# Kernel tuning notes

Hardware: AMD Instinct MI355X
Metric: run time of the kernel (lower is better)

Reference implementation:

```python
import jax, jax.numpy as jnp
import numpy as np

N_NODES = 100000


def _gcn_aggregate(x, edge_index):
    """Symmetric-normalized GCN aggregation with self-loops (PyG gcn_norm).
    Returns A_hat @ x where A_hat = D^-1/2 (A + I) D^-1/2.
    """
    n = x.shape[0]
    row, col = edge_index[0], edge_index[1]          # messages flow row -> col
    loop = jnp.arange(n, dtype=edge_index.dtype)
    src = jnp.concatenate([row, loop])
    dst = jnp.concatenate([col, loop])
    # degree at target nodes (includes self-loop weight 1)
    deg = jax.ops.segment_sum(jnp.ones(src.shape[0], x.dtype), dst, num_segments=n)
    dinv = jnp.where(deg > 0, jax.lax.rsqrt(deg), 0.0)
    coef = dinv[src] * dinv[dst]                     # [E+N]
    msg = x[src] * coef[:, None]                     # [E+N, F] gather + scale
    return jax.ops.segment_sum(msg, dst, num_segments=n)  # [N, F] scatter-add


def setup_inputs() -> dict:
    key = jax.random.key(0)
    k1, k2, k3, k4 = jax.random.split(key, 4)
    in_size, out_size = 128, 64
    n_edges = 3200000
    x = jax.random.normal(k1, (N_NODES, in_size), dtype=jnp.float32)
    edge_index = jax.random.randint(k2, (2, n_edges), 0, N_NODES, dtype=jnp.int32)
    scale = 1.0 / np.sqrt(in_size)
    W_mu = jax.random.normal(k3, (in_size, out_size), dtype=jnp.float32) * scale
    W_logstd = jax.random.normal(k4, (in_size, out_size), dtype=jnp.float32) * scale
    b_mu = jnp.zeros((out_size,), jnp.float32)
    b_logstd = jnp.zeros((out_size,), jnp.float32)
    return {"x": x, "edge_index": edge_index, "W_mu": W_mu, "b_mu": b_mu,
            "W_logstd": W_logstd, "b_logstd": b_logstd}


def reference(x, edge_index, W_mu, b_mu, W_logstd, b_logstd):
    # Both GCNConv branches share the same normalized aggregation; by linearity
    # (A_hat @ x) @ W == A_hat @ (x @ W), so aggregate once and apply each linear.
    agg = _gcn_aggregate(x, edge_index)              # [N, in_size]
    mu = agg @ W_mu + b_mu                           # [N, out_size]
    logstd = agg @ W_logstd + b_logstd               # [N, out_size]
    return (mu, logstd)
```

## Files before the change

### kernel.cpp

```cpp
#include <hip/hip_runtime.h>

#define F_IN 128
#define F_OUT 64
#define TILE 4096
#define CAP 4608

__device__ inline unsigned short f2bf(float f) {
    unsigned int x = __builtin_bit_cast(unsigned int, f);
    unsigned int r = x + 0x7FFFu + ((x >> 16) & 1u);
    return (unsigned short)(r >> 16);
}

__global__ __launch_bounds__(1024) void hist_kernel(
        const int* __restrict__ col, int* __restrict__ cntT, int E, int NB, int NT) {
    __shared__ int h[1024];
    const int t = threadIdx.x;
    const int tile = blockIdx.x;
    const int base = tile * TILE;
    const int n = min(TILE, E - base);
    h[t] = 0;
    __syncthreads();
    const int4* c4 = (const int4*)(col + base);
    const int n4 = n >> 2;
    for (int i = t; i < n4; i += 1024) {
        const int4 c = c4[i];
        atomicAdd(&h[c.x >> 7], 1);
        atomicAdd(&h[c.y >> 7], 1);
        atomicAdd(&h[c.z >> 7], 1);
        atomicAdd(&h[c.w >> 7], 1);
    }
    for (int i = n4 * 4 + t; i < n; i += 1024)
        atomicAdd(&h[col[base + i] >> 7], 1);
    __syncthreads();
    for (int b = t; b < NB; b += 1024)
        cntT[(size_t)tile * NB + b] = h[b];
}

__global__ __launch_bounds__(1024) void scan_kernel(
        const int* __restrict__ cntT, int* __restrict__ gbaseT,
        int* __restrict__ totB, int NB, int NT) {
    __shared__ int wsum[16];
    const int b = blockIdx.x;
    const int t = threadIdx.x;
    const int lane = t & 63;
    const int w = t >> 6;
    const int v = (t < NT) ? cntT[(size_t)t * NB + b] : 0;
    int x = v;
#pragma unroll
    for (int off = 1; off < 64; off <<= 1) {
        const int y = __shfl_up(x, off, 64);
        if (lane >= off) x += y;
    }
    if (lane == 63) wsum[w] = x;
    __syncthreads();
    int add = 0;
    for (int i = 0; i < w; i++) add += wsum[i];
    x += add;
    if (t < NT) gbaseT[(size_t)t * NB + b] = b * CAP + (x - v);
    if (t == 1023) totB[b] = x;
}

__global__ __launch_bounds__(1024) void repack_kernel(
        const int* __restrict__ row, const int* __restrict__ col,
        const int* __restrict__ gbaseT, int* __restrict__ bpk,
        int E, int NB, int NT, int CAPTOT) {
    __shared__ int cur[1024];
    const int t = threadIdx.x;
    const int tile = blockIdx.x;
    const int base = tile * TILE;
    const int n = min(TILE, E - base);
    for (int b = t; b < NB; b += 1024)
        cur[b] = gbaseT[(size_t)tile * NB + b];
    __syncthreads();
    const int4* c4 = (const int4*)(col + base);
    const int4* r4 = (const int4*)(row + base);
    const int n4 = n >> 2;
    for (int i = t; i < n4; i += 1024) {
        const int4 c = c4[i];
        const int4 r = r4[i];
        int p0 = atomicAdd(&cur[c.x >> 7], 1);
        int p1 = atomicAdd(&cur[c.y >> 7], 1);
        int p2 = atomicAdd(&cur[c.z >> 7], 1);
        int p3 = atomicAdd(&cur[c.w >> 7], 1);
        if (p0 < CAPTOT) bpk[p0] = r.x | ((c.x & 127) << 17);
        if (p1 < CAPTOT) bpk[p1] = r.y | ((c.y & 127) << 17);
        if (p2 < CAPTOT) bpk[p2] = r.z | ((c.z & 127) << 17);
        if (p3 < CAPTOT) bpk[p3] = r.w | ((c.w & 127) << 17);
    }
    for (int i = n4 * 4 + t; i < n; i += 1024) {
        const int c = col[base + i];
        const int pos = atomicAdd(&cur[c >> 7], 1);
        if (pos < CAPTOT)
            bpk[pos] = row[base + i] | ((c & 127) << 17);
    }
}

__global__ __launch_bounds__(1024) void deg_kernel(
        const int* __restrict__ bpk, const int* __restrict__ totB,
        int* __restrict__ deg, float* __restrict__ dinv, int N) {
    __shared__ int h[128];
    const int b = blockIdx.x;
    const int t = threadIdx.x;
    if (t < 128) h[t] = 0;
    __syncthreads();
    const int tot = min(totB[b], CAP);
    const int4* bp4 = (const int4*)(bpk + b * CAP);
    const int tot4 = tot >> 2;
    for (int i = t; i < tot4; i += 1024) {
        const int4 v = bp4[i];
        atomicAdd(&h[v.x >> 17], 1);
        atomicAdd(&h[v.y >> 17], 1);
        atomicAdd(&h[v.z >> 17], 1);
        atomicAdd(&h[v.w >> 17], 1);
    }
    for (int i = tot4 * 4 + t; i < tot; i += 1024)
        atomicAdd(&h[bpk[b * CAP + i] >> 17], 1);
    __syncthreads();
    const int node = b * 128 + t;
    if (t < 128 && node < N) {
        deg[node] = h[t];
        dinv[node] = rsqrtf((float)h[t] + 1.0f);
    }
}

__global__ __launch_bounds__(256) void gemm_kernel(
        const float* __restrict__ x, const float* __restrict__ Wmu,
        const float* __restrict__ Wls, const float* __restrict__ dinv,
        unsigned int* __restrict__ y, int N) {
    __shared__ float xs[64 * F_IN];
    const int tid = threadIdx.x;
    const int base = blockIdx.x * 64;
    const int nn = min(64, N - base);
    {
        const float4* xg = (const float4*)(x + (size_t)base * F_IN);
        float4* xs4 = (float4*)xs;
        const int cnt = nn * (F_IN / 4);
        for (int i = tid; i < cnt; i += 256) xs4[i] = xg[i];
    }
    __syncthreads();
    const int wv = tid >> 6;
    const int lane = tid & 63;
    const int half = lane >> 5;
    const int lp = lane & 31;
    const int nbase = wv * 16 + half * 8;
    const float* W0 = (lp < 16) ? Wmu : Wls;
    const int coff = (lp < 16) ? (4 * lp) : (4 * (lp - 16));
    float acc[8][4];
#pragma unroll
    for (int n = 0; n < 8; n++)
#pragma unroll
        for (int c = 0; c < 4; c++) acc[n][c] = 0.f;

    for (int k = 0; k < F_IN; k += 4) {
        const float4 w0 = *(const float4*)&W0[(size_t)(k + 0) * F_OUT + coff];
        const float4 w1 = *(const float4*)&W0[(size_t)(k + 1) * F_OUT + coff];
        const float4 w2 = *(const float4*)&W0[(size_t)(k + 2) * F_OUT + coff];
        const float4 w3 = *(const float4*)&W0[(size_t)(k + 3) * F_OUT + coff];
#pragma unroll
        for (int n = 0; n < 8; n++) {
            const float4 xv = *(const float4*)&xs[(nbase + n) * F_IN + k];
            acc[n][0] = fmaf(xv.x, w0.x, acc[n][0]);
            acc[n][1] = fmaf(xv.x, w0.y, acc[n][1]);
            acc[n][2] = fmaf(xv.x, w0.z, acc[n][2]);
            acc[n][3] = fmaf(xv.x, w0.w, acc[n][3]);
            acc[n][0] = fmaf(xv.y, w1.x, acc[n][0]);
            acc[n][1] = fmaf(xv.y, w1.y, acc[n][1]);
            acc[n][2] = fmaf(xv.y, w1.z, acc[n][2]);
            acc[n][3] = fmaf(xv.y, w1.w, acc[n][3]);
            acc[n][0] = fmaf(xv.z, w2.x, acc[n][0]);
            acc[n][1] = fmaf(xv.z, w2.y, acc[n][1]);
            acc[n][2] = fmaf(xv.z, w2.z, acc[n][2]);
            acc[n][3] = fmaf(xv.z, w2.w, acc[n][3]);
            acc[n][0] = fmaf(xv.w, w3.x, acc[n][0]);
            acc[n][1] = fmaf(xv.w, w3.y, acc[n][1]);
            acc[n][2] = fmaf(xv.w, w3.z, acc[n][2]);
            acc[n][3] = fmaf(xv.w, w3.w, acc[n][3]);
        }
    }
    const int ci = (lp < 16) ? (2 * lp) : (32 + 2 * (lp - 16));
#pragma unroll
    for (int n = 0; n < 8; n++) {
        const int node = base + nbase + n;
        if (node < N) {
            const float dv = dinv[node];
            const unsigned u0 = (unsigned)f2bf(acc[n][0] * dv) |
                                ((unsigned)f2bf(acc[n][1] * dv) << 16);
            const unsigned u1 = (unsigned)f2bf(acc[n][2] * dv) |
                                ((unsigned)f2bf(acc[n][3] * dv) << 16);
            *(uint2*)&y[(size_t)node * 64 + ci] = make_uint2(u0, u1);
        }
    }
}

__global__ __launch_bounds__(1024) void bucket_gather(
        const int* __restrict__ bpk, const int* __restrict__ deg,
        const uint4* __restrict__ Y4,
        const float* __restrict__ bmu, const float* __restrict__ bls,
        float* __restrict__ out, int N) {
    __shared__ int elist[CAP];
    __shared__ int hN[128];
    __shared__ int nodebase[128];
    __shared__ int cursor[128];
    __shared__ float dinv_s[128];
    __shared__ int w0sum;
    const int b = blockIdx.x;
    const int t = threadIdx.x;
    const int lane = t & 63;

    int hv = 0;
    if (t < 128) {
        const int node = b * 128 + t;
        hv = (node < N) ? deg[node] : 0;
        dinv_s[t] = rsqrtf((float)hv + 1.0f);
        hN[t] = hv;
    }
    int x = hv;
#pragma unroll
    for (int off = 1; off < 64; off <<= 1) {
        const int y = __shfl_up(x, off, 64);
        if (lane >= off) x += y;
    }
    if (t == 63) w0sum = x;
    __syncthreads();
    if (t >= 64 && t < 128) x += w0sum;
    if (t < 128) { nodebase[t] = x - hv; cursor[t] = x - hv; }
    __syncthreads();
    const int tot = min(nodebase[127] + hN[127], CAP);

    const int4* bp4 = (const int4*)(bpk + b * CAP);
    const int tot4 = tot >> 2;
    for (int i = t; i < tot4; i += 1024) {
        const int4 v = bp4[i];
        int p0 = atomicAdd(&cursor[v.x >> 17], 1);
        int p1 = atomicAdd(&cursor[v.y >> 17], 1);
        int p2 = atomicAdd(&cursor[v.z >> 17], 1);
        int p3 = atomicAdd(&cursor[v.w >> 17], 1);
        if (p0 < CAP) elist[p0] = v.x & 0x1FFFF;
        if (p1 < CAP) elist[p1] = v.y & 0x1FFFF;
        if (p2 < CAP) elist[p2] = v.z & 0x1FFFF;
        if (p3 < CAP) elist[p3] = v.w & 0x1FFFF;
    }
    for (int i = tot4 * 4 + t; i < tot; i += 1024) {
        const int p = bpk[b * CAP + i];
        const int pos = atomicAdd(&cursor[p >> 17], 1);
        if (pos < CAP) elist[pos] = p & 0x1FFFF;
    }
    __syncthreads();

    const int w = t >> 6;
    const int eg = lane >> 4;
    const int q = lane & 15;

#define ACC(u)                                                        \
    do {                                                              \
        A.x += __builtin_bit_cast(float, (u).x << 16);                \
        A.y += __builtin_bit_cast(float, (u).x & 0xFFFF0000u);        \
        A.z += __builtin_bit_cast(float, (u).y << 16);                \
        A.w += __builtin_bit_cast(float, (u).y & 0xFFFF0000u);        \
        B.x += __builtin_bit_cast(float, (u).z << 16);                \
        B.y += __builtin_bit_cast(float, (u).z & 0xFFFF0000u);        \
        B.z += __builtin_bit_cast(float, (u).w << 16);                \
        B.w += __builtin_bit_cast(float, (u).w & 0xFFFF0000u);        \
    } while (0)

    for (int nid = w * 8; nid < w * 8 + 8; nid++) {
        const int node = b * 128 + nid;
        if (node >= N) continue;
        const int cnt = hN[nid];
        const int nb_ = nodebase[nid];
        float4 A = make_float4(0.f, 0.f, 0.f, 0.f);
        float4 B = make_float4(0.f, 0.f, 0.f, 0.f);
        int e = 0;
        for (; e + 16 <= cnt; e += 16) {
            const int s0 = elist[nb_ + e + 0 + eg];
            const int s1 = elist[nb_ + e + 4 + eg];
            const int s2 = elist[nb_ + e + 8 + eg];
            const int s3 = elist[nb_ + e + 12 + eg];
            const uint4 u0 = Y4[(size_t)s0 * 16 + q];
            const uint4 u1 = Y4[(size_t)s1 * 16 + q];
            const uint4 u2 = Y4[(size_t)s2 * 16 + q];
            const uint4 u3 = Y4[(size_t)s3 * 16 + q];
            ACC(u0); ACC(u1); ACC(u2); ACC(u3);
        }
        for (; e < cnt; e += 4) {
            if (e + eg < cnt) {
                const int s0 = elist[nb_ + e + eg];
                const uint4 u0 = Y4[(size_t)s0 * 16 + q];
                ACC(u0);
            }
        }
        A.x += __shfl_xor(A.x, 16); A.y += __shfl_xor(A.y, 16);
        A.z += __shfl_xor(A.z, 16); A.w += __shfl_xor(A.w, 16);
        B.x += __shfl_xor(B.x, 16); B.y += __shfl_xor(B.y, 16);
        B.z += __shfl_xor(B.z, 16); B.w += __shfl_xor(B.w, 16);
        A.x += __shfl_xor(A.x, 32); A.y += __shfl_xor(A.y, 32);
        A.z += __shfl_xor(A.z, 32); A.w += __shfl_xor(A.w, 32);
        B.x += __shfl_xor(B.x, 32); B.y += __shfl_xor(B.y, 32);
        B.z += __shfl_xor(B.z, 32); B.w += __shfl_xor(B.w, 32);
        {
            const uint4 u = Y4[(size_t)node * 16 + q];
            ACC(u);
        }
        const float dv = dinv_s[nid];
        if (lane < 16) {
            if (q < 8) {
                const float4 b0 = ((const float4*)bmu)[2 * q];
                const float4 b1 = ((const float4*)bmu)[2 * q + 1];
                float* o = out + (size_t)node * F_OUT + q * 8;
                *(float4*)o = make_float4(b0.x + A.x * dv, b0.y + A.y * dv,
                                          b0.z + A.z * dv, b0.w + A.w * dv);
                *(float4*)(o + 4) = make_float4(b1.x + B.x * dv, b1.y + B.y * dv,
                                                b1.z + B.z * dv, b1.w + B.w * dv);
            } else {
                const float4 b0 = ((const float4*)bls)[2 * (q - 8)];
                const float4 b1 = ((const float4*)bls)[2 * (q - 8) + 1];
                float* o = out + ((size_t)N + node) * F_OUT + (q - 8) * 8;
                *(float4*)o = make_float4(b0.x + A.x * dv, b0.y + A.y * dv,
                                          b0.z + A.z * dv, b0.w + A.w * dv);
                *(float4*)(o + 4) = make_float4(b1.x + B.x * dv, b1.y + B.y * dv,
                                                b1.z + B.z * dv, b1.w + B.w * dv);
            }
        }
    }
#undef ACC
}

extern "C" void kernel_launch(void* const* d_in, const int* in_sizes, int n_in,
                              void* d_out, int out_size, void* d_ws, size_t ws_size,
                              hipStream_t stream) {
    const float* x   = (const float*)d_in[0];
    const int*   ei  = (const int*)d_in[1];
    const float* Wmu = (const float*)d_in[2];
    const float* bmu = (const float*)d_in[3];
    const float* Wls = (const float*)d_in[4];
    const float* bls = (const float*)d_in[5];
    float* out = (float*)d_out;

    const int N = in_sizes[0] / F_IN;
    const int E = in_sizes[1] / 2;
    const int* row = ei;
    const int* col = ei + E;
    const int NB = (N + 127) >> 7;
    const int NT = (E + TILE - 1) / TILE;
    const int CAPTOT = NB * CAP;

    char* p = (char*)d_ws;
    auto alloc = [&](size_t bytes) {
        char* r = p;
        p += (bytes + 511) & ~(size_t)511;
        return r;
    };
    int*   cntT   = (int*)  alloc((size_t)NT * NB * 4);
    int*   gbaseT = (int*)  alloc((size_t)NT * NB * 4);
    int*   totB   = (int*)  alloc((size_t)NB * 4);
    int*   bpk    = (int*)  alloc((size_t)CAPTOT * 4 + 4096);
    int*   deg    = (int*)  alloc((size_t)N * 4);
    float* dinv   = (float*)alloc((size_t)N * 4);
    unsigned int* y = (unsigned int*)alloc((size_t)N * F_IN * 2);

    hist_kernel<<<NT, 1024, 0, stream>>>(col, cntT, E, NB, NT);
    scan_kernel<<<NB, 1024, 0, stream>>>(cntT, gbaseT, totB, NB, NT);
    repack_kernel<<<NT, 1024, 0, stream>>>(row, col, gbaseT, bpk, E, NB, NT, CAPTOT);
    deg_kernel<<<NB, 1024, 0, stream>>>(bpk, totB, deg, dinv, N);
    gemm_kernel<<<(N + 63) / 64, 256, 0, stream>>>(x, Wmu, Wls, dinv, y, N);
    bucket_gather<<<NB, 1024, 0, stream>>>(bpk, deg, (const uint4*)y,
                                           bmu, bls, out, N);
}
```

Measured before the change: 328.9 us.

## Replace histogram+scan+repack with single-pass repack using global atomic bucket cursors

Merges the per-tile histogram, cross-tile prefix scan and repack kernels into one kernel. Each tile histograms its column indices in shared memory, reserves space in each destination bucket with one global atomicAdd per bucket, then scatters packed edges. This removes two kernel launches, the cntT/gbaseT round trips and one extra read of the column array, since columns are cached in LDS. In exchange, edge order within a bucket is now nondeterministic, which may change floating-point summation order, and the per-bucket overflow check now uses the bucket bound.

```diff
diff --git a/kernel.cpp b/kernel.cpp
--- a/kernel.cpp
+++ b/kernel.cpp
@@ -11,87 +11,65 @@
     return (unsigned short)(r >> 16);
 }
 
-__global__ __launch_bounds__(1024) void hist_kernel(
-        const int* __restrict__ col, int* __restrict__ cntT, int E, int NB, int NT) {
-    __shared__ int h[1024];
-    const int t = threadIdx.x;
-    const int tile = blockIdx.x;
-    const int base = tile * TILE;
-    const int n = min(TILE, E - base);
-    h[t] = 0;
-    __syncthreads();
-    const int4* c4 = (const int4*)(col + base);
-    const int n4 = n >> 2;
-    for (int i = t; i < n4; i += 1024) {
-        const int4 c = c4[i];
-        atomicAdd(&h[c.x >> 7], 1);
-        atomicAdd(&h[c.y >> 7], 1);
-        atomicAdd(&h[c.z >> 7], 1);
-        atomicAdd(&h[c.w >> 7], 1);
-    }
-    for (int i = n4 * 4 + t; i < n; i += 1024)
-        atomicAdd(&h[col[base + i] >> 7], 1);
-    __syncthreads();
-    for (int b = t; b < NB; b += 1024)
-        cntT[(size_t)tile * NB + b] = h[b];
-}
-
-__global__ __launch_bounds__(1024) void scan_kernel(
-        const int* __restrict__ cntT, int* __restrict__ gbaseT,
-        int* __restrict__ totB, int NB, int NT) {
-    __shared__ int wsum[16];
-    const int b = blockIdx.x;
-    const int t = threadIdx.x;
-    const int lane = t & 63;
-    const int w = t >> 6;
-    const int v = (t < NT) ? cntT[(size_t)t * NB + b] : 0;
-    int x = v;
-#pragma unroll
-    for (int off = 1; off < 64; off <<= 1) {
-        const int y = __shfl_up(x, off, 64);
-        if (lane >= off) x += y;
-    }
-    if (lane == 63) wsum[w] = x;
-    __syncthreads();
-    int add = 0;
-    for (int i = 0; i < w; i++) add += wsum[i];
-    x += add;
-    if (t < NT) gbaseT[(size_t)t * NB + b] = b * CAP + (x - v);
-    if (t == 1023) totB[b] = x;
-}
-
-__global__ __launch_bounds__(1024) void repack_kernel(
+__global__ __launch_bounds__(1024) void repack_dyn(
         const int* __restrict__ row, const int* __restrict__ col,
-        const int* __restrict__ gbaseT, int* __restrict__ bpk,
-        int E, int NB, int NT, int CAPTOT) {
+        int* __restrict__ gcur, int* __restrict__ bpk, int E, int NB) {
+    __shared__ __align__(16) int colbuf[TILE];
     __shared__ int cur[1024];
     const int t = threadIdx.x;
     const int tile = blockIdx.x;
     const int base = tile * TILE;
     const int n = min(TILE, E - base);
-    for (int b = t; b < NB; b += 1024)
-        cur[b] = gbaseT[(size_t)tile * NB + b];
-    __syncthreads();
-    const int4* c4 = (const int4*)(col + base);
-    const int4* r4 = (const int4*)(row + base);
     const int n4 = n >> 2;
-    for (int i = t; i < n4; i += 1024) {
-        const int4 c = c4[i];
-        const int4 r = r4[i];
-        int p0 = atomicAdd(&cur[c.x >> 7], 1);
-        int p1 = atomicAdd(&cur[c.y >> 7], 1);
-        int p2 = atomicAdd(&cur[c.z >> 7], 1);
-        int p3 = atomicAdd(&cur[c.w >> 7], 1);
-        if (p0 < CAPTOT) bpk[p0] = r.x | ((c.x & 127) << 17);
-        if (p1 < CAPTOT) bpk[p1] = r.y | ((c.y & 127) << 17);
-        if (p2 < CAPTOT) bpk[p2] = r.z | ((c.z & 127) << 17);
-        if (p3 < CAPTOT) bpk[p3] = r.w | ((c.w & 127) << 17);
-    }
-    for (int i = n4 * 4 + t; i < n; i += 1024) {
-        const int c = col[base + i];
-        const int pos = atomicAdd(&cur[c >> 7], 1);
-        if (pos < CAPTOT)
-            bpk[pos] = row[base + i] | ((c & 127) << 17);
+    cur[t] = 0;
+    __syncthreads();
+    {
+        const int4* c4 = (const int4*)(col + base);
+        for (int i = t; i < n4; i += 1024) {
+            const int4 c = c4[i];
+            *(int4*)&colbuf[4 * i] = c;
+            atomicAdd(&cur[c.x >> 7], 1);
+            atomicAdd(&cur[c.y >> 7], 1);
+            atomicAdd(&cur[c.z >> 7], 1);
+            atomicAdd(&cur[c.w >> 7], 1);
+        }
+        for (int i = n4 * 4 + t; i < n; i += 1024) {
+            const int c = col[base + i];
+            colbuf[i] = c;
+            atomicAdd(&cur[c >> 7], 1);
+        }
+    }
+    __syncthreads();
+    {
+        const int h = cur[t];
+        int rb = 0;
+        if (t < NB && h > 0) rb = atomicAdd(&gcur[t], h);
+        cur[t] = t * CAP + rb;
+    }
+    __syncthreads();
+    {
+        const int4* r4 = (const int4*)(row + base);
+        for (int i = t; i < n4; i += 1024) {
+            const int4 r = r4[i];
+            const int cx = colbuf[4 * i + 0];
+            const int cy = colbuf[4 * i + 1];
+            const int cz = colbuf[4 * i + 2];
+            const int cw = colbuf[4 * i + 3];
+            const int p0 = atomicAdd(&cur[cx >> 7], 1);
+            const int p1 = atomicAdd(&cur[cy >> 7], 1);
+            const int p2 = atomicAdd(&cur[cz >> 7], 1);
+            const int p3 = atomicAdd(&cur[cw >> 7], 1);
+            if (p0 < (cx >> 7) * CAP + CAP) bpk[p0] = r.x | ((cx & 127) << 17);
+            if (p1 < (cy >> 7) * CAP + CAP) bpk[p1] = r.y | ((cy & 127) << 17);
+            if (p2 < (cz >> 7) * CAP + CAP) bpk[p2] = r.z | ((cz & 127) << 17);
+            if (p3 < (cw >> 7) * CAP + CAP) bpk[p3] = r.w | ((cw & 127) << 17);
+        }
+        for (int i = n4 * 4 + t; i < n; i += 1024) {
+            const int c = colbuf[i];
+            const int pos = atomicAdd(&cur[c >> 7], 1);
+            if (pos < (c >> 7) * CAP + CAP)
+                bpk[pos] = row[base + i] | ((c & 127) << 17);
+        }
     }
 }
 
@@ -127,7 +105,7 @@
         const float* __restrict__ x, const float* __restrict__ Wmu,
         const float* __restrict__ Wls, const float* __restrict__ dinv,
         unsigned int* __restrict__ y, int N) {
-    __shared__ float xs[64 * F_IN];
+    __shared__ __align__(16) float xs[64 * F_IN];
     const int tid = threadIdx.x;
     const int base = blockIdx.x * 64;
     const int nn = min(64, N - base);
@@ -350,18 +328,15 @@
         p += (bytes + 511) & ~(size_t)511;
         return r;
     };
-    int*   cntT   = (int*)  alloc((size_t)NT * NB * 4);
-    int*   gbaseT = (int*)  alloc((size_t)NT * NB * 4);
-    int*   totB   = (int*)  alloc((size_t)NB * 4);
-    int*   bpk    = (int*)  alloc((size_t)CAPTOT * 4 + 4096);
-    int*   deg    = (int*)  alloc((size_t)N * 4);
-    float* dinv   = (float*)alloc((size_t)N * 4);
+    int*   gcur  = (int*)  alloc((size_t)NB * 4);
+    int*   bpk   = (int*)  alloc((size_t)CAPTOT * 4 + 4096);
+    int*   deg   = (int*)  alloc((size_t)N * 4);
+    float* dinv  = (float*)alloc((size_t)N * 4);
     unsigned int* y = (unsigned int*)alloc((size_t)N * F_IN * 2);
 
-    hist_kernel<<<NT, 1024, 0, stream>>>(col, cntT, E, NB, NT);
-    scan_kernel<<<NB, 1024, 0, stream>>>(cntT, gbaseT, totB, NB, NT);
-    repack_kernel<<<NT, 1024, 0, stream>>>(row, col, gbaseT, bpk, E, NB, NT, CAPTOT);
-    deg_kernel<<<NB, 1024, 0, stream>>>(bpk, totB, deg, dinv, N);
+    hipMemsetAsync(gcur, 0, (size_t)NB * 4, stream);
+    repack_dyn<<<NT, 1024, 0, stream>>>(row, col, gcur, bpk, E, NB);
+    deg_kernel<<<NB, 1024, 0, stream>>>(bpk, gcur, deg, dinv, N);
     gemm_kernel<<<(N + 63) / 64, 256, 0, stream>>>(x, Wmu, Wls, dinv, y, N);
     bucket_gather<<<NB, 1024, 0, stream>>>(bpk, deg, (const uint4*)y,
                                            bmu, bls, out, N);
```

New measurement: 319.3 us (median of 2 runs). 1.03x faster.
